# Performance work log

Measured on AMD Instinct MI355X. Metric: run time of the kernel, lower is better.

The kernel has to match this reference:

```python
import jax, jax.numpy as jnp
import numpy as np

B, S, D, H = 2, 2048, 2048, 16
HD = D // H  # head_dim = 128


def setup_inputs() -> dict:
    key = jax.random.key(0)
    k1, k2, k3, k4, k5, k6 = jax.random.split(key, 6)
    scale = 1.0 / np.sqrt(D)
    return {
        "hidden_states": jax.random.normal(k1, (B, S, D), dtype=jnp.float32),
        "attention_mask": jnp.ones((B, S), dtype=jnp.int32),
        "wq": jax.random.normal(k2, (D, D), dtype=jnp.float32) * scale,
        "wk": jax.random.normal(k3, (D, D), dtype=jnp.float32) * scale,
        "wv": jax.random.normal(k4, (D, D), dtype=jnp.float32) * scale,
        "wo": jax.random.normal(k5, (D, D), dtype=jnp.float32) * scale,
        "bo": jax.random.normal(k6, (D,), dtype=jnp.float32) * 0.01,
    }


def reference(hidden_states, attention_mask, wq, wk, wv, wo, bo):
    b, s, d = hidden_states.shape
    # QKV projections (no bias), split heads -> [B, S, H, HD]
    q = (hidden_states @ wq).reshape(b, s, H, HD)
    k = (hidden_states @ wk).reshape(b, s, H, HD)
    v = (hidden_states @ wv).reshape(b, s, H, HD)

    # combined causal + padding mask -> [B, 1, S, S]
    causal = jnp.tril(jnp.ones((s, s), dtype=bool))[None, None]
    pad = (attention_mask > 0)[:, None, None, :]  # [B,1,1,S]
    mask = jnp.logical_and(causal, pad)

    big_neg = jnp.finfo(hidden_states.dtype).min
    bias = jnp.where(mask, 0.0, big_neg).astype(hidden_states.dtype)

    # scaled dot-product attention (flax dot_product_attention scales by 1/sqrt(head_dim))
    scores = jnp.einsum("bqhd,bkhd->bhqk", q, k) / jnp.sqrt(jnp.asarray(HD, hidden_states.dtype))
    probs = jax.nn.softmax(scores + bias, axis=-1)
    ctx = jnp.einsum("bhqk,bkhd->bqhd", probs, v).reshape(b, s, d)

    return ctx @ wo + bo
```

## Files before the change

### kernel.cpp

```cpp
#include <hip/hip_runtime.h>
#include <hip/hip_bf16.h>
#include <stdint.h>

#define Bv 2
#define Sv 2048
#define Dv 2048
#define Hv 16
#define HDv 128
#define Mv (Bv*Sv)

typedef __attribute__((ext_vector_type(8))) short short8;
typedef __attribute__((ext_vector_type(4))) short short4v;
typedef __attribute__((ext_vector_type(4))) float f32x4;

__device__ __forceinline__ unsigned short bf16_rne(float f) {
    union { float f; uint32_t u; } c; c.f = f;
    uint32_t u = c.u;
    u += 0x7fffu + ((u >> 16) & 1u);
    return (unsigned short)(u >> 16);
}

__device__ __forceinline__ uint32_t cvt_pk_bf16(float lo, float hi) {
    uint32_t r;
    asm("v_cvt_pk_bf16_f32 %0, %1, %2" : "=v"(r) : "v"(lo), "v"(hi));
    return r;
}

__device__ __forceinline__ void gload16(const void* g, void* l) {
    __builtin_amdgcn_global_load_lds((const __attribute__((address_space(1))) void*)g,
                                     (__attribute__((address_space(3))) void*)l, 16, 0, 0);
}

__global__ void cvt_x_kernel(const float* __restrict__ x, unsigned short* __restrict__ xb) {
    int i = (blockIdx.x * 256 + threadIdx.x) * 4;
    float4 v = *(const float4*)(x + i);
    short4v o;
    o[0] = (short)bf16_rne(v.x);
    o[1] = (short)bf16_rne(v.y);
    o[2] = (short)bf16_rne(v.z);
    o[3] = (short)bf16_rne(v.w);
    *(short4v*)(xb + i) = o;
}

__global__ void cvt_wt_kernel(const float* __restrict__ w0, const float* __restrict__ w1,
                              const float* __restrict__ w2, const float* __restrict__ w3,
                              unsigned short* __restrict__ wt) {
    __shared__ unsigned short t[64][65];
    int z = blockIdx.z;
    const float* w = (z == 0) ? w0 : (z == 1) ? w1 : (z == 2) ? w2 : w3;
    unsigned short* o = wt + (size_t)z * Dv * Dv;
    int k0 = blockIdx.x * 64, n0 = blockIdx.y * 64;
    for (int i = threadIdx.x; i < 4096; i += 256) {
        int r = i >> 6, c = i & 63;
        t[r][c] = bf16_rne(w[(size_t)(k0 + r) * Dv + n0 + c]);
    }
    __syncthreads();
    for (int i = threadIdx.x; i < 4096; i += 256) {
        int r = i >> 6, c = i & 63;
        o[(size_t)(n0 + r) * Dv + k0 + c] = t[c][r];
    }
}

__global__ void vt_kernel(const unsigned short* __restrict__ V, unsigned short* __restrict__ VT) {
    __shared__ unsigned short t[64 * 64];
    const int tid = threadIdx.x;
    const int b = blockIdx.z;
    const int s0 = blockIdx.x * 64, c0 = blockIdx.y * 64;
    const unsigned short* Vb = V + (size_t)b * Sv * Dv;
    unsigned short* VTb = VT + (size_t)b * Dv * Sv;
    #pragma unroll
    for (int ii = 0; ii < 2; ++ii) {
        int i = tid + ii * 256;
        int r = i >> 3, ch = i & 7;
        short8 v = *(const short8*)&Vb[(size_t)(s0 + r) * Dv + c0 + ch * 8];
        *(short8*)&t[r * 64 + ((ch ^ (r & 7)) << 3)] = v;
    }
    __syncthreads();
    #pragma unroll
    for (int ii = 0; ii < 2; ++ii) {
        int o = tid + ii * 256;
        int orow = o >> 3, och = o & 7;
        short8 v;
        #pragma unroll
        for (int j = 0; j < 8; ++j) {
            int r = och * 8 + j;
            int c = orow;
            v[j] = (short)t[r * 64 + ((((c >> 3) ^ (r & 7)) << 3) | (c & 7))];
        }
        *(short8*)&VTb[(size_t)(c0 + orow) * Sv + s0 + och * 8] = v;
    }
}

template<int FOUT>
__global__ __launch_bounds__(512, 2) void gemm8_kernel(
    const unsigned short* __restrict__ A,
    const unsigned short* __restrict__ WtBase,
    unsigned short* __restrict__ CbBase,
    float* __restrict__ Cf,
    const float* __restrict__ bias,
    int per_xcd_n)
{
    extern __shared__ unsigned short lds[];
    const int tid = threadIdx.x;
    const int wv = tid >> 6, ln = tid & 63;
    const int lr = ln & 15, lg = ln >> 4;
    const int wm = wv >> 2, wn = wv & 3;

    const int bid = blockIdx.x;
    const int xcd = bid & 7, idx = bid >> 3;
    const int n_idx = xcd * per_xcd_n + (idx >> 5);
    const int m_idx = idx & 31;
    const int m0 = m_idx * 128;
    const int n0g = n_idx * 256;
    const int NT = Dv / 64;

    const int srow = ln >> 3;
    const int swz = ((ln & 7) ^ srow) << 3;
    const unsigned short* Ab = A      + (size_t)(m0  + wv * 8 + srow) * Dv + swz;
    const unsigned short* Bb = WtBase + (size_t)(n0g + wv * 8 + srow) * Dv + swz;

    auto STAGE_A = [&](int t, int d) {
        const unsigned short* g = Ab + t * 64;
        #pragma unroll
        for (int j = 0; j < 2; ++j)
            gload16(g + (size_t)(j * 64) * Dv, &lds[d * 24576 + (j * 64 + wv * 8) * 64]);
    };
    auto STAGE_B = [&](int t, int d) {
        const unsigned short* g = Bb + t * 64;
        #pragma unroll
        for (int j = 0; j < 4; ++j)
            gload16(g + (size_t)(j * 64) * Dv, &lds[d * 24576 + 8192 + (j * 64 + wv * 8) * 64]);
    };

    const int aro = (wm * 64 + lr) * 64;
    const int bro = (wn * 64 + lr) * 64;
    const int ach0 = ((lg ^ (lr & 7)) << 3);
    const int ach1 = (((4 + lg) ^ (lr & 7)) << 3);

    f32x4 acc[4][4];
    #pragma unroll
    for (int mi = 0; mi < 4; mi++)
        #pragma unroll
        for (int ni = 0; ni < 4; ni++)
            acc[mi][ni] = (f32x4){0.f, 0.f, 0.f, 0.f};

    STAGE_A(0, 0); STAGE_B(0, 0);
    STAGE_A(1, 1); STAGE_B(1, 1);
    asm volatile("s_waitcnt vmcnt(6)" ::: "memory");
    asm volatile("s_barrier" ::: "memory");

    for (int t = 0; t < NT; ++t) {
        const int d = t % 3, d2 = (t + 2) % 3;
        const unsigned short* la = &lds[d * 24576];
        const unsigned short* lb = &lds[d * 24576 + 8192];

        short8 af[4][2], bf0[2][2];
        #pragma unroll
        for (int mi = 0; mi < 4; mi++) {
            af[mi][0] = *(const short8*)&la[aro + mi * 1024 + ach0];
            af[mi][1] = *(const short8*)&la[aro + mi * 1024 + ach1];
        }
        #pragma unroll
        for (int ni = 0; ni < 2; ni++) {
            bf0[ni][0] = *(const short8*)&lb[bro + ni * 1024 + ach0];
            bf0[ni][1] = *(const short8*)&lb[bro + ni * 1024 + ach1];
        }
        if (t + 2 < NT) STAGE_A(t + 2, d2);
        asm volatile("s_barrier" ::: "memory");
        __builtin_amdgcn_s_setprio(1);
        #pragma unroll
        for (int mi = 0; mi < 4; mi++)
            #pragma unroll
            for (int ni = 0; ni < 2; ni++) {
                acc[mi][ni] = __builtin_amdgcn_mfma_f32_16x16x32_bf16(af[mi][0], bf0[ni][0], acc[mi][ni], 0, 0, 0);
                acc[mi][ni] = __builtin_amdgcn_mfma_f32_16x16x32_bf16(af[mi][1], bf0[ni][1], acc[mi][ni], 0, 0, 0);
            }
        __builtin_amdgcn_s_setprio(0);

        short8 bf1[2][2];
        #pragma unroll
        for (int ni = 0; ni < 2; ni++) {
            bf1[ni][0] = *(const short8*)&lb[bro + (ni + 2) * 1024 + ach0];
            bf1[ni][1] = *(const short8*)&lb[bro + (ni + 2) * 1024 + ach1];
        }
        if (t + 2 < NT) STAGE_B(t + 2, d2);
        asm volatile("s_waitcnt vmcnt(6)" ::: "memory");
        asm volatile("s_barrier" ::: "memory");
        __builtin_amdgcn_s_setprio(1);
        #pragma unroll
        for (int mi = 0; mi < 4; mi++)
            #pragma unroll
            for (int ni = 0; ni < 2; ni++) {
                acc[mi][ni + 2] = __builtin_amdgcn_mfma_f32_16x16x32_bf16(af[mi][0], bf1[ni][0], acc[mi][ni + 2], 0, 0, 0);
                acc[mi][ni + 2] = __builtin_amdgcn_mfma_f32_16x16x32_bf16(af[mi][1], bf1[ni][1], acc[mi][ni + 2], 0, 0, 0);
            }
        __builtin_amdgcn_s_setprio(0);
    }

    if (FOUT) {
        #pragma unroll
        for (int mi = 0; mi < 4; mi++)
            #pragma unroll
            for (int ni = 0; ni < 4; ni++) {
                int row = m0 + wm * 64 + mi * 16 + lg * 4;
                int col = n0g + wn * 64 + ni * 16 + lr;
                float bv = bias[col];
                #pragma unroll
                for (int r = 0; r < 4; r++)
                    Cf[(size_t)(row + r) * Dv + col] = acc[mi][ni][r] + bv;
            }
    } else {
        const int z = n0g >> 11;
        unsigned short* Cz = CbBase + (size_t)z * Mv * Dv;
        const int ncl = (n0g & 2047) + wn * 64;
        #pragma unroll
        for (int mi = 0; mi < 4; mi++)
            #pragma unroll
            for (int ni = 0; ni < 4; ni++) {
                int row = m0 + wm * 64 + mi * 16 + lg * 4;
                int col = ncl + ni * 16 + lr;
                #pragma unroll
                for (int r = 0; r < 4; r++)
                    Cz[(size_t)(row + r) * Dv + col] = bf16_rne(acc[mi][ni][r]);
            }
    }
}

__global__ __launch_bounds__(512) void attn_kernel(
    const unsigned short* __restrict__ Q, const unsigned short* __restrict__ K,
    const unsigned short* __restrict__ VT, const int* __restrict__ pmask,
    unsigned short* __restrict__ CTX)
{
    __shared__ unsigned short lK[2][64 * 128];
    __shared__ unsigned short lVt[2][128 * 64];
    __shared__ int lPmB[2][64];
    __shared__ int lPmOk[2];

    const int tid = threadIdx.x, wv = tid >> 6, ln = tid & 63;
    const int lr = ln & 15, lg = ln >> 4;
    const int L = blockIdx.x;
    const int bh = (L & 7) * 4 + ((L >> 3) & 3);
    const int b = bh >> 4, h = bh & 15;
    const int v = L >> 5;
    const int qidx = (v < 8) ? (15 - v) : (v - 8);
    const int q0 = qidx * 128;
    const int qw0 = q0 + wv * 16;
    const size_t hoff  = (size_t)b * Sv * Dv + (size_t)h * HDv;
    const size_t vtoff = ((size_t)b * Dv + (size_t)h * HDv) * Sv;

    short8 qf[4];
    #pragma unroll
    for (int ds = 0; ds < 4; ds++)
        qf[ds] = *(const short8*)&Q[hoff + (size_t)(qw0 + lr) * Dv + ds * 32 + lg * 8];

    size_t koff[2], voff[2];
    #pragma unroll
    for (int ii = 0; ii < 2; ++ii) {
        int slot = ii * 512 + wv * 64 + ln;
        int krow = slot >> 4, kch = slot & 15;
        koff[ii] = hoff + (size_t)krow * Dv + ((kch ^ (krow & 7)) << 3);
        int vrow = slot >> 3, vch = slot & 7;
        voff[ii] = vtoff + (size_t)vrow * Sv + ((vch ^ (vrow & 7)) << 3);
    }

    auto STAGE = [&](int t, int buf) {
        const size_t kadd = (size_t)(t << 6) * Dv;
        const int vadd = t << 6;
        unsigned short* kb = &lK[buf][0];
        unsigned short* vb = &lVt[buf][0];
        #pragma unroll
        for (int ii = 0; ii < 2; ++ii) {
            gload16(K + koff[ii] + kadd, kb + (ii * 512 + wv * 64) * 8);
            gload16(VT + voff[ii] + vadd, vb + (ii * 512 + wv * 64) * 8);
        }
        if (wv == 0) {
            int pmv = pmask[b * Sv + (t << 6) + ln];
            lPmB[buf][ln] = pmv;
            unsigned long long bal = __ballot(pmv != 0);
            if (ln == 0) lPmOk[buf] = (bal == ~0ull) ? 1 : 0;
        }
    };

    f32x4 acc[8];
    #pragma unroll
    for (int n = 0; n < 8; n++) acc[n] = (f32x4){0.f, 0.f, 0.f, 0.f};
    float mrow = -3.0e38f, lrow = 0.f;
    const float CS = 0.12751744f;
    const int qg = qw0 + lr;
    const int nt = (q0 >> 6) + 2;
    const int srcA = lr + ((lg & 1) << 5);
    const int srcB = srcA + 16;
    const bool hiSel = (lg >= 2);

    auto TILE = [&](int t, int buf, auto CAUSAL_c) {
        constexpr bool CAUSAL = decltype(CAUSAL_c)::value;
        const int kv0 = t << 6;
        const unsigned short* kb = &lK[buf][0];
        const unsigned short* vb = &lVt[buf][0];

        f32x4 st[4];
        #pragma unroll
        for (int t2 = 0; t2 < 4; ++t2) st[t2] = (f32x4){0.f, 0.f, 0.f, 0.f};
        __builtin_amdgcn_s_setprio(1);
        #pragma unroll
        for (int t2 = 0; t2 < 4; ++t2) {
            const int krow = t2 * 16 + lr;
            #pragma unroll
            for (int ds = 0; ds < 4; ++ds) {
                const int ch = ds * 4 + lg;
                short8 kf = *(const short8*)&kb[krow * 128 + ((ch ^ (krow & 7)) << 3)];
                st[t2] = __builtin_amdgcn_mfma_f32_16x16x32_bf16(kf, qf[ds], st[t2], 0, 0, 0);
            }
        }
        __builtin_amdgcn_s_setprio(0);

        float sv[4][4];
        float rmax;
        if constexpr (CAUSAL) {
            const int* pm = &lPmB[buf][0];
            #pragma unroll
            for (int t2 = 0; t2 < 4; ++t2)
                #pragma unroll
                for (int r = 0; r < 4; ++r) {
                    int kvl = t2 * 16 + lg * 4 + r;
                    bool ok = ((kv0 + kvl) <= qg) && (pm[kvl] != 0);
                    sv[t2][r] = ok ? st[t2][r] * CS : -1.0e30f;
                }
            rmax = sv[0][0];
            #pragma unroll
            for (int t2 = 0; t2 < 4; ++t2)
                #pragma unroll
                for (int r = 0; r < 4; ++r) rmax = fmaxf(rmax, sv[t2][r]);
            rmax = fmaxf(rmax, __shfl_xor(rmax, 16, 64));
            rmax = fmaxf(rmax, __shfl_xor(rmax, 32, 64));
        } else {
            rmax = st[0][0];
            #pragma unroll
            for (int t2 = 0; t2 < 4; ++t2)
                #pragma unroll
                for (int r = 0; r < 4; ++r) rmax = fmaxf(rmax, st[t2][r]);
            rmax = fmaxf(rmax, __shfl_xor(rmax, 16, 64));
            rmax = fmaxf(rmax, __shfl_xor(rmax, 32, 64));
            rmax *= CS;
        }

        if (!__all(rmax - mrow <= 8.0f)) {
            float mn = fmaxf(mrow, rmax);
            float alpha = exp2f(mrow - mn);
            mrow = mn;
            lrow *= alpha;
            #pragma unroll
            for (int n = 0; n < 8; n++)
                #pragma unroll
                for (int r = 0; r < 4; r++) acc[n][r] *= alpha;
        }

        float p[4][4]; float psum = 0.f;
        if constexpr (CAUSAL) {
            #pragma unroll
            for (int t2 = 0; t2 < 4; ++t2)
                #pragma unroll
                for (int r = 0; r < 4; ++r) {
                    float e = exp2f(sv[t2][r] - mrow);
                    p[t2][r] = (sv[t2][r] > -5.0e29f) ? e : 0.f;
                    psum += p[t2][r];
                }
        } else {
            if (lPmOk[buf]) {
                #pragma unroll
                for (int t2 = 0; t2 < 4; ++t2)
                    #pragma unroll
                    for (int r = 0; r < 4; ++r) {
                        p[t2][r] = exp2f(fmaf(st[t2][r], CS, -mrow));
                        psum += p[t2][r];
                    }
            } else {
                const int* pm = &lPmB[buf][0];
                #pragma unroll
                for (int t2 = 0; t2 < 4; ++t2)
                    #pragma unroll
                    for (int r = 0; r < 4; ++r) {
                        int kvl = t2 * 16 + lg * 4 + r;
                        float e = exp2f(fmaf(st[t2][r], CS, -mrow));
                        p[t2][r] = (pm[kvl] != 0) ? e : 0.f;
                        psum += p[t2][r];
                    }
            }
        }
        psum += __shfl_xor(psum, 16, 64);
        psum += __shfl_xor(psum, 32, 64);
        lrow += psum;

        uint32_t pk[4][2];
        #pragma unroll
        for (int t2 = 0; t2 < 4; ++t2)
            #pragma unroll
            for (int pp = 0; pp < 2; ++pp)
                pk[t2][pp] = cvt_pk_bf16(p[t2][2 * pp], p[t2][2 * pp + 1]);

        union U { uint32_t u[4]; short8 s; } pa0, pa1;
        {
            uint32_t l0 = (uint32_t)__shfl((int)pk[0][0], srcA, 64), h0 = (uint32_t)__shfl((int)pk[1][0], srcA, 64);
            uint32_t l1 = (uint32_t)__shfl((int)pk[0][1], srcA, 64), h1 = (uint32_t)__shfl((int)pk[1][1], srcA, 64);
            uint32_t l2 = (uint32_t)__shfl((int)pk[0][0], srcB, 64), h2 = (uint32_t)__shfl((int)pk[1][0], srcB, 64);
            uint32_t l3 = (uint32_t)__shfl((int)pk[0][1], srcB, 64), h3 = (uint32_t)__shfl((int)pk[1][1], srcB, 64);
            pa0.u[0] = hiSel ? h0 : l0; pa0.u[1] = hiSel ? h1 : l1;
            pa0.u[2] = hiSel ? h2 : l2; pa0.u[3] = hiSel ? h3 : l3;
        }
        {
            uint32_t l0 = (uint32_t)__shfl((int)pk[2][0], srcA, 64), h0 = (uint32_t)__shfl((int)pk[3][0], srcA, 64);
            uint32_t l1 = (uint32_t)__shfl((int)pk[2][1], srcA, 64), h1 = (uint32_t)__shfl((int)pk[3][1], srcA, 64);
            uint32_t l2 = (uint32_t)__shfl((int)pk[2][0], srcB, 64), h2 = (uint32_t)__shfl((int)pk[3][0], srcB, 64);
            uint32_t l3 = (uint32_t)__shfl((int)pk[2][1], srcB, 64), h3 = (uint32_t)__shfl((int)pk[3][1], srcB, 64);
            pa1.u[0] = hiSel ? h0 : l0; pa1.u[1] = hiSel ? h1 : l1;
            pa1.u[2] = hiSel ? h2 : l2; pa1.u[3] = hiSel ? h3 : l3;
        }

        __builtin_amdgcn_s_setprio(1);
        #pragma unroll
        for (int n = 0; n < 8; n++) {
            const int vrow = n * 16 + lr;
            short8 a0 = *(const short8*)&vb[vrow * 64 + ((lg ^ (vrow & 7)) << 3)];
            acc[n] = __builtin_amdgcn_mfma_f32_16x16x32_bf16(a0, pa0.s, acc[n], 0, 0, 0);
            short8 a1 = *(const short8*)&vb[vrow * 64 + (((4 + lg) ^ (vrow & 7)) << 3)];
            acc[n] = __builtin_amdgcn_mfma_f32_16x16x32_bf16(a1, pa1.s, acc[n], 0, 0, 0);
        }
        __builtin_amdgcn_s_setprio(0);
    };

    STAGE(0, 0);
    __syncthreads();
    int cur = 0;

    for (int t = 0; t < nt; ++t) {
        if (t + 1 < nt) STAGE(t + 1, cur ^ 1);
        const int kv0 = t << 6;
        if (kv0 <= qw0 + 15) {
            if (kv0 + 63 > qw0) TILE(t, cur, std::integral_constant<bool, true>{});
            else                TILE(t, cur, std::integral_constant<bool, false>{});
        }
        __syncthreads();
        cur ^= 1;
    }

    float inv = 1.0f / lrow;
    #pragma unroll
    for (int n = 0; n < 8; n++) {
        short4v o;
        #pragma unroll
        for (int r = 0; r < 4; r++) o[r] = (short)bf16_rne(acc[n][r] * inv);
        *(short4v*)&CTX[hoff + (size_t)qg * Dv + n * 16 + lg * 4] = o;
    }
}

extern "C" void kernel_launch(void* const* d_in, const int* in_sizes, int n_in,
                              void* d_out, int out_size, void* d_ws, size_t ws_size,
                              hipStream_t stream) {
    const float* hs  = (const float*)d_in[0];
    const int*   am  = (const int*)d_in[1];
    const float* wq  = (const float*)d_in[2];
    const float* wk  = (const float*)d_in[3];
    const float* wv_ = (const float*)d_in[4];
    const float* wo  = (const float*)d_in[5];
    const float* bo  = (const float*)d_in[6];
    float* out = (float*)d_out;

    char* ws = (char*)d_ws;
    unsigned short* Xb  = (unsigned short*)ws;
    unsigned short* Wt  = (unsigned short*)(ws + (size_t)16 * 1024 * 1024);
    unsigned short* QKV = (unsigned short*)(ws + (size_t)48 * 1024 * 1024);
    unsigned short* CTX = (unsigned short*)(ws + (size_t)96 * 1024 * 1024);
    unsigned short* VT  = Xb;

    const int LDSB = 3 * 24576 * 2;
    static bool attrSet = false;
    if (!attrSet) {
        hipFuncSetAttribute((const void*)gemm8_kernel<0>, hipFuncAttributeMaxDynamicSharedMemorySize, LDSB);
        hipFuncSetAttribute((const void*)gemm8_kernel<1>, hipFuncAttributeMaxDynamicSharedMemorySize, LDSB);
        attrSet = true;
    }

    hipLaunchKernelGGL(cvt_x_kernel, dim3(Mv * Dv / 4 / 256), dim3(256), 0, stream, hs, Xb);
    hipLaunchKernelGGL(cvt_wt_kernel, dim3(32, 32, 4), dim3(256), 0, stream, wq, wk, wv_, wo, Wt);
    hipLaunchKernelGGL(gemm8_kernel<0>, dim3(768), dim3(512), LDSB, stream,
                       Xb, Wt, QKV, (float*)nullptr, (const float*)nullptr, 3);
    hipLaunchKernelGGL(vt_kernel, dim3(32, 32, 2), dim3(256), 0, stream,
                       QKV + 2 * (size_t)Mv * Dv, VT);
    hipLaunchKernelGGL(attn_kernel, dim3(512), dim3(512), 0, stream,
                       QKV, QKV + (size_t)Mv * Dv, VT, am, CTX);
    hipLaunchKernelGGL(gemm8_kernel<1>, dim3(256), dim3(512), LDSB, stream,
                       CTX, Wt + 3 * (size_t)Dv * Dv, (unsigned short*)nullptr, out, bo, 1);
}
```

Before: 243.1 us.

## Restructure GEMM to 256x256 tiles with K=32 stages, templated on M-block

Replaces the 128x256 GEMM tile with a templated kernel. The QKV projection now uses 256x256 tiles (384 blocks instead of 768), while the output projection keeps 128x256. Each stage now covers K=32 instead of K=64, with a new LDS layout and 4-chunk swizzle. Larger tiles raise arithmetic intensity and cut how often A and B are reloaded, but they double the accumulators for QKV, which risks register pressure and lower occupancy, and the shorter K stages add more barriers per unit of work.

```diff
diff --git a/kernel.cpp b/kernel.cpp
--- a/kernel.cpp
+++ b/kernel.cpp
@@ -91,16 +91,21 @@
     }
 }
 
-template<int FOUT>
-__global__ __launch_bounds__(512, 2) void gemm8_kernel(
+template<int FOUT, int MB>
+__global__ __launch_bounds__(512, 2) void gemm256_kernel(
     const unsigned short* __restrict__ A,
     const unsigned short* __restrict__ WtBase,
     unsigned short* __restrict__ CbBase,
     float* __restrict__ Cf,
     const float* __restrict__ bias,
-    int per_xcd_n)
+    int n_per_xcd, int m_cnt)
 {
+    constexpr int BM   = MB * 32;
+    constexpr int AISS = BM / 128;
+    constexpr int SLOT = (BM + 256) * 32;
+    constexpr int IPT  = AISS + 2;
     extern __shared__ unsigned short lds[];
+
     const int tid = threadIdx.x;
     const int wv = tid >> 6, ln = tid & 63;
     const int lr = ln & 15, lg = ln >> 4;
@@ -108,120 +113,106 @@
 
     const int bid = blockIdx.x;
     const int xcd = bid & 7, idx = bid >> 3;
-    const int n_idx = xcd * per_xcd_n + (idx >> 5);
-    const int m_idx = idx & 31;
-    const int m0 = m_idx * 128;
-    const int n0g = n_idx * 256;
-    const int NT = Dv / 64;
-
-    const int srow = ln >> 3;
-    const int swz = ((ln & 7) ^ srow) << 3;
-    const unsigned short* Ab = A      + (size_t)(m0  + wv * 8 + srow) * Dv + swz;
-    const unsigned short* Bb = WtBase + (size_t)(n0g + wv * 8 + srow) * Dv + swz;
-
-    auto STAGE_A = [&](int t, int d) {
-        const unsigned short* g = Ab + t * 64;
+    const int n_idx = xcd * n_per_xcd + idx / m_cnt;
+    const int m_idx = idx % m_cnt;
+    const int m0 = m_idx * BM, n0g = n_idx * 256;
+    const int NT = Dv / 32;
+
+    const int srow = tid >> 2;
+    const int swzc = ((tid & 3) ^ (srow & 3)) << 3;
+    const unsigned short* Ab = A      + (size_t)(m0  + srow) * Dv + swzc;
+    const unsigned short* Bb = WtBase + (size_t)(n0g + srow) * Dv + swzc;
+
+    auto STAGE_A = [&](int t, int s) {
+        #pragma unroll
+        for (int j = 0; j < AISS; ++j)
+            gload16(Ab + (size_t)(j * 128) * Dv + t * 32, &lds[s * SLOT + (j * 512 + wv * 64) * 8]);
+    };
+    auto STAGE_B = [&](int t, int s) {
         #pragma unroll
         for (int j = 0; j < 2; ++j)
-            gload16(g + (size_t)(j * 64) * Dv, &lds[d * 24576 + (j * 64 + wv * 8) * 64]);
+            gload16(Bb + (size_t)(j * 128) * Dv + t * 32, &lds[s * SLOT + BM * 32 + (j * 512 + wv * 64) * 8]);
     };
-    auto STAGE_B = [&](int t, int d) {
-        const unsigned short* g = Bb + t * 64;
-        #pragma unroll
-        for (int j = 0; j < 4; ++j)
-            gload16(g + (size_t)(j * 64) * Dv, &lds[d * 24576 + 8192 + (j * 64 + wv * 8) * 64]);
-    };
-
-    const int aro = (wm * 64 + lr) * 64;
-    const int bro = (wn * 64 + lr) * 64;
-    const int ach0 = ((lg ^ (lr & 7)) << 3);
-    const int ach1 = (((4 + lg) ^ (lr & 7)) << 3);
-
-    f32x4 acc[4][4];
-    #pragma unroll
-    for (int mi = 0; mi < 4; mi++)
-        #pragma unroll
-        for (int ni = 0; ni < 4; ni++)
-            acc[mi][ni] = (f32x4){0.f, 0.f, 0.f, 0.f};
+
+    const int rch = (lg ^ (lr & 3)) << 3;
+    const int arow0 = wm * (MB * 16) + lr;
+    const int brow0 = wn * 64 + lr;
+
+    f32x4 acc[MB][4];
+    #pragma unroll
+    for (int fm = 0; fm < MB; fm++)
+        #pragma unroll
+        for (int fn = 0; fn < 4; fn++)
+            acc[fm][fn] = (f32x4){0.f, 0.f, 0.f, 0.f};
 
     STAGE_A(0, 0); STAGE_B(0, 0);
     STAGE_A(1, 1); STAGE_B(1, 1);
-    asm volatile("s_waitcnt vmcnt(6)" ::: "memory");
+    asm volatile("s_waitcnt vmcnt(%0)" :: "i"(IPT) : "memory");
     asm volatile("s_barrier" ::: "memory");
 
     for (int t = 0; t < NT; ++t) {
-        const int d = t % 3, d2 = (t + 2) % 3;
-        const unsigned short* la = &lds[d * 24576];
-        const unsigned short* lb = &lds[d * 24576 + 8192];
-
-        short8 af[4][2], bf0[2][2];
-        #pragma unroll
-        for (int mi = 0; mi < 4; mi++) {
-            af[mi][0] = *(const short8*)&la[aro + mi * 1024 + ach0];
-            af[mi][1] = *(const short8*)&la[aro + mi * 1024 + ach1];
-        }
-        #pragma unroll
-        for (int ni = 0; ni < 2; ni++) {
-            bf0[ni][0] = *(const short8*)&lb[bro + ni * 1024 + ach0];
-            bf0[ni][1] = *(const short8*)&lb[bro + ni * 1024 + ach1];
-        }
-        if (t + 2 < NT) STAGE_A(t + 2, d2);
+        const int s = t % 3, s2 = (t + 2) % 3;
+        const unsigned short* la = &lds[s * SLOT];
+        const unsigned short* lb = &lds[s * SLOT + BM * 32];
+
+        short8 a4[4], b4[4];
+        #pragma unroll
+        for (int f = 0; f < 4; ++f) a4[f] = *(const short8*)&la[(arow0 + f * 16) * 32 + rch];
+        #pragma unroll
+        for (int f = 0; f < 4; ++f) b4[f] = *(const short8*)&lb[(brow0 + f * 16) * 32 + rch];
+        if (t + 2 < NT) { STAGE_A(t + 2, s2); if (MB == 4) STAGE_B(t + 2, s2); }
+        if (MB == 4) asm volatile("s_waitcnt vmcnt(%0)" :: "i"(IPT) : "memory");
         asm volatile("s_barrier" ::: "memory");
         __builtin_amdgcn_s_setprio(1);
         #pragma unroll
-        for (int mi = 0; mi < 4; mi++)
-            #pragma unroll
-            for (int ni = 0; ni < 2; ni++) {
-                acc[mi][ni] = __builtin_amdgcn_mfma_f32_16x16x32_bf16(af[mi][0], bf0[ni][0], acc[mi][ni], 0, 0, 0);
-                acc[mi][ni] = __builtin_amdgcn_mfma_f32_16x16x32_bf16(af[mi][1], bf0[ni][1], acc[mi][ni], 0, 0, 0);
-            }
+        for (int fm = 0; fm < 4; ++fm)
+            #pragma unroll
+            for (int fn = 0; fn < 4; ++fn)
+                acc[fm][fn] = __builtin_amdgcn_mfma_f32_16x16x32_bf16(a4[fm], b4[fn], acc[fm][fn], 0, 0, 0);
         __builtin_amdgcn_s_setprio(0);
 
-        short8 bf1[2][2];
-        #pragma unroll
-        for (int ni = 0; ni < 2; ni++) {
-            bf1[ni][0] = *(const short8*)&lb[bro + (ni + 2) * 1024 + ach0];
-            bf1[ni][1] = *(const short8*)&lb[bro + (ni + 2) * 1024 + ach1];
-        }
-        if (t + 2 < NT) STAGE_B(t + 2, d2);
-        asm volatile("s_waitcnt vmcnt(6)" ::: "memory");
-        asm volatile("s_barrier" ::: "memory");
-        __builtin_amdgcn_s_setprio(1);
-        #pragma unroll
-        for (int mi = 0; mi < 4; mi++)
-            #pragma unroll
-            for (int ni = 0; ni < 2; ni++) {
-                acc[mi][ni + 2] = __builtin_amdgcn_mfma_f32_16x16x32_bf16(af[mi][0], bf1[ni][0], acc[mi][ni + 2], 0, 0, 0);
-                acc[mi][ni + 2] = __builtin_amdgcn_mfma_f32_16x16x32_bf16(af[mi][1], bf1[ni][1], acc[mi][ni + 2], 0, 0, 0);
-            }
-        __builtin_amdgcn_s_setprio(0);
+        if (MB == 8) {
+            short8 a8[4];
+            #pragma unroll
+            for (int f = 0; f < 4; ++f) a8[f] = *(const short8*)&la[(arow0 + (4 + f) * 16) * 32 + rch];
+            if (t + 2 < NT) STAGE_B(t + 2, s2);
+            asm volatile("s_waitcnt vmcnt(%0)" :: "i"(IPT) : "memory");
+            asm volatile("s_barrier" ::: "memory");
+            __builtin_amdgcn_s_setprio(1);
+            #pragma unroll
+            for (int fm = 0; fm < 4; ++fm)
+                #pragma unroll
+                for (int fn = 0; fn < 4; ++fn)
+                    acc[4 + fm][fn] = __builtin_amdgcn_mfma_f32_16x16x32_bf16(a8[fm], b4[fn], acc[4 + fm][fn], 0, 0, 0);
+            __builtin_amdgcn_s_setprio(0);
+        }
     }
 
     if (FOUT) {
         #pragma unroll
-        for (int mi = 0; mi < 4; mi++)
-            #pragma unroll
-            for (int ni = 0; ni < 4; ni++) {
-                int row = m0 + wm * 64 + mi * 16 + lg * 4;
-                int col = n0g + wn * 64 + ni * 16 + lr;
+        for (int fm = 0; fm < MB; fm++)
+            #pragma unroll
+            for (int fn = 0; fn < 4; fn++) {
+                int row = m0 + wm * (MB * 16) + fm * 16 + lg * 4;
+                int col = n0g + wn * 64 + fn * 16 + lr;
                 float bv = bias[col];
                 #pragma unroll
                 for (int r = 0; r < 4; r++)
-                    Cf[(size_t)(row + r) * Dv + col] = acc[mi][ni][r] + bv;
+                    Cf[(size_t)(row + r) * Dv + col] = acc[fm][fn][r] + bv;
             }
     } else {
         const int z = n0g >> 11;
         unsigned short* Cz = CbBase + (size_t)z * Mv * Dv;
         const int ncl = (n0g & 2047) + wn * 64;
         #pragma unroll
-        for (int mi = 0; mi < 4; mi++)
-            #pragma unroll
-            for (int ni = 0; ni < 4; ni++) {
-                int row = m0 + wm * 64 + mi * 16 + lg * 4;
-                int col = ncl + ni * 16 + lr;
+        for (int fm = 0; fm < MB; fm++)
+            #pragma unroll
+            for (int fn = 0; fn < 4; fn++) {
+                int row = m0 + wm * (MB * 16) + fm * 16 + lg * 4;
+                int col = ncl + fn * 16 + lr;
                 #pragma unroll
                 for (int r = 0; r < 4; r++)
-                    Cz[(size_t)(row + r) * Dv + col] = bf16_rne(acc[mi][ni][r]);
+                    Cz[(size_t)(row + r) * Dv + col] = bf16_rne(acc[fm][fn][r]);
             }
     }
 }
@@ -472,22 +463,23 @@
     unsigned short* CTX = (unsigned short*)(ws + (size_t)96 * 1024 * 1024);
     unsigned short* VT  = Xb;
 
-    const int LDSB = 3 * 24576 * 2;
+    const int LDSB_QKV = 3 * (256 + 256) * 32 * 2;
+    const int LDSB_OUT = 3 * (128 + 256) * 32 * 2;
     static bool attrSet = false;
     if (!attrSet) {
-        hipFuncSetAttribute((const void*)gemm8_kernel<0>, hipFuncAttributeMaxDynamicSharedMemorySize, LDSB);
-        hipFuncSetAttribute((const void*)gemm8_kernel<1>, hipFuncAttributeMaxDynamicSharedMemorySize, LDSB);
+        hipFuncSetAttribute((const void*)gemm256_kernel<0, 8>, hipFuncAttributeMaxDynamicSharedMemorySize, LDSB_QKV);
+        hipFuncSetAttribute((const void*)gemm256_kernel<1, 4>, hipFuncAttributeMaxDynamicSharedMemorySize, LDSB_OUT);
         attrSet = true;
     }
 
     hipLaunchKernelGGL(cvt_x_kernel, dim3(Mv * Dv / 4 / 256), dim3(256), 0, stream, hs, Xb);
     hipLaunchKernelGGL(cvt_wt_kernel, dim3(32, 32, 4), dim3(256), 0, stream, wq, wk, wv_, wo, Wt);
-    hipLaunchKernelGGL(gemm8_kernel<0>, dim3(768), dim3(512), LDSB, stream,
-                       Xb, Wt, QKV, (float*)nullptr, (const float*)nullptr, 3);
+    hipLaunchKernelGGL((gemm256_kernel<0, 8>), dim3(384), dim3(512), LDSB_QKV, stream,
+                       Xb, Wt, QKV, (float*)nullptr, (const float*)nullptr, 3, 16);
     hipLaunchKernelGGL(vt_kernel, dim3(32, 32, 2), dim3(256), 0, stream,
                        QKV + 2 * (size_t)Mv * Dv, VT);
     hipLaunchKernelGGL(attn_kernel, dim3(512), dim3(512), 0, stream,
                        QKV, QKV + (size_t)Mv * Dv, VT, am, CTX);
-    hipLaunchKernelGGL(gemm8_kernel<1>, dim3(256), dim3(512), LDSB, stream,
-                       CTX, Wt + 3 * (size_t)Dv * Dv, (unsigned short*)nullptr, out, bo, 1);
-}
+    hipLaunchKernelGGL((gemm256_kernel<1, 4>), dim3(256), dim3(512), LDSB_OUT, stream,
+                       CTX, Wt + 3 * (size_t)Dv * Dv, (unsigned short*)nullptr, out, bo, 1, 32);
+}
```

New measurement: 262.6 us. 8.0% more time.

## Use 256x256-tile eight-phase pipelined GEMM for QKV projection

Applied to the files above, without the earlier changes.

Replaces the QKV projection GEMM (128x256 tiles, triple-buffered) with a dedicated kernel using 256x256 output tiles, double-buffered LDS split into half-tile loads, and an eight-phase schedule that interleaves LDS reads, global-to-LDS prefetches and MFMA blocks behind barriers. Larger tiles raise arithmetic intensity and halve the block count to 384. This aims to cut global/LDS traffic per FLOP and hide load latency. The trade-offs are 128 accumulator registers per lane, many more barriers, and 128 KB of LDS per block, which limits occupancy. The output GEMM is de-templated, and its LDS attribute is raised to 144 KB although it still uses about the same buffers.

```diff
diff --git a/kernel.cpp b/kernel.cpp
--- a/kernel.cpp
+++ b/kernel.cpp
@@ -30,6 +30,10 @@
     __builtin_amdgcn_global_load_lds((const __attribute__((address_space(1))) void*)g,
                                      (__attribute__((address_space(3))) void*)l, 16, 0, 0);
 }
+
+#define BARRIER() asm volatile("s_barrier" ::: "memory")
+#define LGKM0()   do { asm volatile("s_waitcnt lgkmcnt(0)" ::: "memory"); \
+                       __builtin_amdgcn_sched_barrier(0); } while (0)
 
 __global__ void cvt_x_kernel(const float* __restrict__ x, unsigned short* __restrict__ xb) {
     int i = (blockIdx.x * 256 + threadIdx.x) * 4;
@@ -91,14 +95,10 @@
     }
 }
 
-template<int FOUT>
-__global__ __launch_bounds__(512, 2) void gemm8_kernel(
+__global__ __launch_bounds__(512, 2) void gemm8ph_kernel(
     const unsigned short* __restrict__ A,
     const unsigned short* __restrict__ WtBase,
-    unsigned short* __restrict__ CbBase,
-    float* __restrict__ Cf,
-    const float* __restrict__ bias,
-    int per_xcd_n)
+    unsigned short* __restrict__ CbBase)
 {
     extern __shared__ unsigned short lds[];
     const int tid = threadIdx.x;
@@ -108,8 +108,153 @@
 
     const int bid = blockIdx.x;
     const int xcd = bid & 7, idx = bid >> 3;
-    const int n_idx = xcd * per_xcd_n + (idx >> 5);
-    const int m_idx = idx & 31;
+    const int n_idx = xcd * 3 + idx / 16;
+    const int m_idx = idx % 16;
+    const int m0 = m_idx * 256, n0g = n_idx * 256;
+
+    const int lrow = wv * 8 + (ln >> 3);
+    const int lcol = ((ln & 7) ^ (ln >> 3)) << 3;
+    const unsigned short* Ag = A      + (size_t)(m0  + lrow) * Dv + lcol;
+    const unsigned short* Bg = WtBase + (size_t)(n0g + lrow) * Dv + lcol;
+
+    auto SH = [&](int T, int isB, int h) {
+        const unsigned short* src = (isB ? Bg : Ag) + (size_t)(h * 128) * Dv + T * 64;
+        unsigned short* dst = &lds[(T & 1) * 32768 + isB * 16384 + h * 8192 + wv * 512];
+        gload16(src, dst);
+        gload16(src + (size_t)64 * Dv, dst + 4096);
+    };
+
+    const int axk = lr & 7;
+    auto RDA = [&](int buf, int fm, int ks) {
+        return *(const short8*)&lds[buf * 32768 + (wm * 128 + fm * 16 + lr) * 64 + (((ks * 4 + lg) ^ axk) << 3)];
+    };
+    auto RDB = [&](int buf, int fn, int ks) {
+        return *(const short8*)&lds[buf * 32768 + 16384 + (wn * 64 + fn * 16 + lr) * 64 + (((ks * 4 + lg) ^ axk) << 3)];
+    };
+
+    f32x4 acc[8][4];
+    #pragma unroll
+    for (int fm = 0; fm < 8; fm++)
+        #pragma unroll
+        for (int fn = 0; fn < 4; fn++)
+            acc[fm][fn] = (f32x4){0.f, 0.f, 0.f, 0.f};
+
+    SH(0, 0, 0); SH(0, 0, 1); SH(0, 1, 0); SH(0, 1, 1);
+    SH(1, 1, 0); SH(1, 0, 0);
+    asm volatile("s_waitcnt vmcnt(4)" ::: "memory");
+    BARRIER();
+
+    short8 af[8], b0[4], b1[4];
+    const int NT2 = 16;
+
+    #define MFMA_BLK(FN0, FN1, BARR) do {                                              \
+        __builtin_amdgcn_s_setprio(1);                                                 \
+        _Pragma("unroll")                                                              \
+        for (int fm = 0; fm < 8; fm++) {                                               \
+            acc[fm][FN0] = __builtin_amdgcn_mfma_f32_16x16x32_bf16(af[fm], BARR[FN0], acc[fm][FN0], 0, 0, 0); \
+            acc[fm][FN1] = __builtin_amdgcn_mfma_f32_16x16x32_bf16(af[fm], BARR[FN1], acc[fm][FN1], 0, 0, 0); \
+        }                                                                              \
+        __builtin_amdgcn_s_setprio(0);                                                 \
+    } while (0)
+
+    for (int i = 0; i < NT2; ++i) {
+        const int Tb = 2 * i + 1;
+        const bool more = (i + 1 < NT2);
+
+        #pragma unroll
+        for (int fm = 0; fm < 8; fm++) af[fm] = RDA(0, fm, 0);
+        #pragma unroll
+        for (int fn = 0; fn < 4; fn++) b0[fn] = RDB(0, fn, 0);
+        SH(Tb, 0, 1);
+        BARRIER(); LGKM0();
+        MFMA_BLK(0, 1, b0);
+        BARRIER();
+
+        #pragma unroll
+        for (int fn = 0; fn < 4; fn++) b1[fn] = RDB(0, fn, 1);
+        SH(Tb, 1, 1);
+        BARRIER(); LGKM0();
+        MFMA_BLK(2, 3, b0);
+        BARRIER();
+
+        #pragma unroll
+        for (int fm = 0; fm < 8; fm++) af[fm] = RDA(0, fm, 1);
+        if (more) SH(Tb + 1, 1, 0);
+        BARRIER(); LGKM0();
+        MFMA_BLK(0, 1, b1);
+        BARRIER();
+
+        if (more) SH(Tb + 1, 0, 0);
+        BARRIER(); LGKM0();
+        MFMA_BLK(2, 3, b1);
+        if (more) asm volatile("s_waitcnt vmcnt(4)" ::: "memory");
+        else      asm volatile("s_waitcnt vmcnt(0)" ::: "memory");
+        BARRIER();
+
+        #pragma unroll
+        for (int fm = 0; fm < 8; fm++) af[fm] = RDA(1, fm, 0);
+        #pragma unroll
+        for (int fn = 0; fn < 4; fn++) b0[fn] = RDB(1, fn, 0);
+        if (more) SH(Tb + 1, 0, 1);
+        BARRIER(); LGKM0();
+        MFMA_BLK(0, 1, b0);
+        BARRIER();
+
+        #pragma unroll
+        for (int fn = 0; fn < 4; fn++) b1[fn] = RDB(1, fn, 1);
+        if (more) SH(Tb + 1, 1, 1);
+        BARRIER(); LGKM0();
+        MFMA_BLK(2, 3, b0);
+        BARRIER();
+
+        #pragma unroll
+        for (int fm = 0; fm < 8; fm++) af[fm] = RDA(1, fm, 1);
+        if (more) SH(Tb + 2, 1, 0);
+        BARRIER(); LGKM0();
+        MFMA_BLK(0, 1, b1);
+        BARRIER();
+
+        if (more) SH(Tb + 2, 0, 0);
+        BARRIER(); LGKM0();
+        MFMA_BLK(2, 3, b1);
+        if (more) {
+            asm volatile("s_waitcnt vmcnt(4)" ::: "memory");
+            BARRIER();
+        }
+    }
+    #undef MFMA_BLK
+
+    const int z = n0g >> 11;
+    unsigned short* Cz = CbBase + (size_t)z * Mv * Dv;
+    const int ncl = (n0g & 2047) + wn * 64;
+    #pragma unroll
+    for (int fm = 0; fm < 8; fm++)
+        #pragma unroll
+        for (int fn = 0; fn < 4; fn++) {
+            int row = m0 + wm * 128 + fm * 16 + lg * 4;
+            int col = ncl + fn * 16 + lr;
+            #pragma unroll
+            for (int r = 0; r < 4; r++)
+                Cz[(size_t)(row + r) * Dv + col] = bf16_rne(acc[fm][fn][r]);
+        }
+}
+
+__global__ __launch_bounds__(512, 2) void gemm8_kernel(
+    const unsigned short* __restrict__ A,
+    const unsigned short* __restrict__ WtBase,
+    float* __restrict__ Cf,
+    const float* __restrict__ bias)
+{
+    extern __shared__ unsigned short lds[];
+    const int tid = threadIdx.x;
+    const int wv = tid >> 6, ln = tid & 63;
+    const int lr = ln & 15, lg = ln >> 4;
+    const int wm = wv >> 2, wn = wv & 3;
+
+    const int bid = blockIdx.x;
+    const int xcd = bid & 7, idx = bid >> 3;
+    const int n_idx = xcd;
+    const int m_idx = idx;
     const int m0 = m_idx * 128;
     const int n0g = n_idx * 256;
     const int NT = Dv / 64;
@@ -147,7 +292,7 @@
     STAGE_A(0, 0); STAGE_B(0, 0);
     STAGE_A(1, 1); STAGE_B(1, 1);
     asm volatile("s_waitcnt vmcnt(6)" ::: "memory");
-    asm volatile("s_barrier" ::: "memory");
+    BARRIER();
 
     for (int t = 0; t < NT; ++t) {
         const int d = t % 3, d2 = (t + 2) % 3;
@@ -166,7 +311,7 @@
             bf0[ni][1] = *(const short8*)&lb[bro + ni * 1024 + ach1];
         }
         if (t + 2 < NT) STAGE_A(t + 2, d2);
-        asm volatile("s_barrier" ::: "memory");
+        BARRIER();
         __builtin_amdgcn_s_setprio(1);
         #pragma unroll
         for (int mi = 0; mi < 4; mi++)
@@ -185,7 +330,7 @@
         }
         if (t + 2 < NT) STAGE_B(t + 2, d2);
         asm volatile("s_waitcnt vmcnt(6)" ::: "memory");
-        asm volatile("s_barrier" ::: "memory");
+        BARRIER();
         __builtin_amdgcn_s_setprio(1);
         #pragma unroll
         for (int mi = 0; mi < 4; mi++)
@@ -197,33 +342,17 @@
         __builtin_amdgcn_s_setprio(0);
     }
 
-    if (FOUT) {
-        #pragma unroll
-        for (int mi = 0; mi < 4; mi++)
-            #pragma unroll
-            for (int ni = 0; ni < 4; ni++) {
-                int row = m0 + wm * 64 + mi * 16 + lg * 4;
-                int col = n0g + wn * 64 + ni * 16 + lr;
-                float bv = bias[col];
-                #pragma unroll
-                for (int r = 0; r < 4; r++)
-                    Cf[(size_t)(row + r) * Dv + col] = acc[mi][ni][r] + bv;
-            }
-    } else {
-        const int z = n0g >> 11;
-        unsigned short* Cz = CbBase + (size_t)z * Mv * Dv;
-        const int ncl = (n0g & 2047) + wn * 64;
-        #pragma unroll
-        for (int mi = 0; mi < 4; mi++)
-            #pragma unroll
-            for (int ni = 0; ni < 4; ni++) {
-                int row = m0 + wm * 64 + mi * 16 + lg * 4;
-                int col = ncl + ni * 16 + lr;
-                #pragma unroll
-                for (int r = 0; r < 4; r++)
-                    Cz[(size_t)(row + r) * Dv + col] = bf16_rne(acc[mi][ni][r]);
-            }
-    }
+    #pragma unroll
+    for (int mi = 0; mi < 4; mi++)
+        #pragma unroll
+        for (int ni = 0; ni < 4; ni++) {
+            int row = m0 + wm * 64 + mi * 16 + lg * 4;
+            int col = n0g + wn * 64 + ni * 16 + lr;
+            float bv = bias[col];
+            #pragma unroll
+            for (int r = 0; r < 4; r++)
+                Cf[(size_t)(row + r) * Dv + col] = acc[mi][ni][r] + bv;
+        }
 }
 
 __global__ __launch_bounds__(512) void attn_kernel(
@@ -472,22 +601,22 @@
     unsigned short* CTX = (unsigned short*)(ws + (size_t)96 * 1024 * 1024);
     unsigned short* VT  = Xb;
 
-    const int LDSB = 3 * 24576 * 2;
+    const int LDSB_8PH = 131072;
+    const int LDSB_OUT = 147456;
     static bool attrSet = false;
     if (!attrSet) {
-        hipFuncSetAttribute((const void*)gemm8_kernel<0>, hipFuncAttributeMaxDynamicSharedMemorySize, LDSB);
-        hipFuncSetAttribute((const void*)gemm8_kernel<1>, hipFuncAttributeMaxDynamicSharedMemorySize, LDSB);
+        hipFuncSetAttribute((const void*)gemm8ph_kernel, hipFuncAttributeMaxDynamicSharedMemorySize, LDSB_8PH);
+        hipFuncSetAttribute((const void*)gemm8_kernel, hipFuncAttributeMaxDynamicSharedMemorySize, LDSB_OUT);
         attrSet = true;
     }
 
     hipLaunchKernelGGL(cvt_x_kernel, dim3(Mv * Dv / 4 / 256), dim3(256), 0, stream, hs, Xb);
     hipLaunchKernelGGL(cvt_wt_kernel, dim3(32, 32, 4), dim3(256), 0, stream, wq, wk, wv_, wo, Wt);
-    hipLaunchKernelGGL(gemm8_kernel<0>, dim3(768), dim3(512), LDSB, stream,
-                       Xb, Wt, QKV, (float*)nullptr, (const float*)nullptr, 3);
+    hipLaunchKernelGGL(gemm8ph_kernel, dim3(384), dim3(512), LDSB_8PH, stream, Xb, Wt, QKV);
     hipLaunchKernelGGL(vt_kernel, dim3(32, 32, 2), dim3(256), 0, stream,
                        QKV + 2 * (size_t)Mv * Dv, VT);
     hipLaunchKernelGGL(attn_kernel, dim3(512), dim3(512), 0, stream,
                        QKV, QKV + (size_t)Mv * Dv, VT, am, CTX);
-    hipLaunchKernelGGL(gemm8_kernel<1>, dim3(256), dim3(512), LDSB, stream,
-                       CTX, Wt + 3 * (size_t)Dv * Dv, (unsigned short*)nullptr, out, bo, 1);
-}
+    hipLaunchKernelGGL(gemm8_kernel, dim3(256), dim3(512), LDSB_OUT, stream,
+                       CTX, Wt + 3 * (size_t)Dv * Dv, out, bo);
+}
```

New measurement: 249.9 us. +2.8%, slower.

## Add dedicated 256-thread QKV GEMM kernel with K=32 triple-buffered tiles

Applied to the files above, without the earlier changes.

Replaces the templated QKV projection GEMM with a new 4-wave kernel. It uses 128x256 tiles with a K-step of 32 and a 3-slot LDS ring of 72KB, so more blocks can be resident per CU. Each wave computes 128x64 with 8x4 MFMA fragments, and there is one barrier pair per K-step. The output GEMM is specialized to the fp32+bias path. Risks include higher register pressure from 32 accumulators, more loop iterations and barriers, and narrower per-wave B reuse.

```diff
diff --git a/kernel.cpp b/kernel.cpp
--- a/kernel.cpp
+++ b/kernel.cpp
@@ -30,6 +30,10 @@
     __builtin_amdgcn_global_load_lds((const __attribute__((address_space(1))) void*)g,
                                      (__attribute__((address_space(3))) void*)l, 16, 0, 0);
 }
+
+#define BARRIER() asm volatile("s_barrier" ::: "memory")
+#define LGKM0()   do { asm volatile("s_waitcnt lgkmcnt(0)" ::: "memory"); \
+                       __builtin_amdgcn_sched_barrier(0); } while (0)
 
 __global__ void cvt_x_kernel(const float* __restrict__ x, unsigned short* __restrict__ xb) {
     int i = (blockIdx.x * 256 + threadIdx.x) * 4;
@@ -91,14 +95,109 @@
     }
 }
 
-template<int FOUT>
+__global__ __launch_bounds__(256, 2) void gemmP_kernel(
+    const unsigned short* __restrict__ A,
+    const unsigned short* __restrict__ WtBase,
+    unsigned short* __restrict__ CbBase)
+{
+    extern __shared__ unsigned short lds[];
+    constexpr int SLOT = 12288;
+    constexpr int BOFF = 4096;
+    constexpr int NT = Dv / 32;
+
+    const int tid = threadIdx.x;
+    const int wv = tid >> 6, ln = tid & 63;
+    const int lr = ln & 15, lg = ln >> 4;
+
+    const int bid = blockIdx.x;
+    const int xcd = bid & 7, idx = bid >> 3;
+    const int n_idx = xcd * 3 + idx / 32;
+    const int m_idx = idx % 32;
+    const int m0 = m_idx * 128, n0g = n_idx * 256;
+
+    const int srow = wv * 16 + (ln >> 2);
+    const int scol = (((ln & 3) ^ ((srow >> 2) & 3)) << 3);
+    const unsigned short* Ag = A      + (size_t)(m0  + srow) * Dv + scol;
+    const unsigned short* Bg = WtBase + (size_t)(n0g + srow) * Dv + scol;
+
+    auto SA = [&](int t, int j) {
+        gload16(Ag + (size_t)(j * 64) * Dv + t * 32,
+                &lds[(t % 3) * SLOT + j * 2048 + wv * 512]);
+    };
+    auto SB = [&](int t, int j) {
+        gload16(Bg + (size_t)(j * 64) * Dv + t * 32,
+                &lds[(t % 3) * SLOT + BOFF + j * 2048 + wv * 512]);
+    };
+
+    auto RDA = [&](int d, int fm) {
+        int row = fm * 16 + lr;
+        return *(const short8*)&lds[d * SLOT + row * 32 + ((lg ^ ((row >> 2) & 3)) << 3)];
+    };
+    auto RDB = [&](int d, int fn) {
+        int row = wv * 64 + fn * 16 + lr;
+        return *(const short8*)&lds[d * SLOT + BOFF + row * 32 + ((lg ^ ((row >> 2) & 3)) << 3)];
+    };
+
+    f32x4 acc[8][4];
+    #pragma unroll
+    for (int fm = 0; fm < 8; fm++)
+        #pragma unroll
+        for (int fn = 0; fn < 4; fn++)
+            acc[fm][fn] = (f32x4){0.f, 0.f, 0.f, 0.f};
+
+    SA(0, 0); SA(0, 1); SB(0, 0); SB(0, 1); SB(0, 2); SB(0, 3);
+    SA(1, 0); SA(1, 1); SB(1, 0); SB(1, 1); SB(1, 2); SB(1, 3);
+    asm volatile("s_waitcnt vmcnt(6)" ::: "memory");
+    BARRIER();
+
+    for (int t = 0; t < NT; ++t) {
+        const int d = t % 3;
+
+        short8 af[8], b[4];
+        #pragma unroll
+        for (int fm = 0; fm < 8; fm++) af[fm] = RDA(d, fm);
+        #pragma unroll
+        for (int fn = 0; fn < 4; fn++) b[fn] = RDB(d, fn);
+
+        if (t + 2 < NT) {
+            SA(t + 2, 0); SA(t + 2, 1);
+            SB(t + 2, 0); SB(t + 2, 1); SB(t + 2, 2); SB(t + 2, 3);
+        }
+        BARRIER(); LGKM0();
+
+        __builtin_amdgcn_s_setprio(1);
+        #pragma unroll
+        for (int fm = 0; fm < 8; fm++)
+            #pragma unroll
+            for (int fn = 0; fn < 4; fn++)
+                acc[fm][fn] = __builtin_amdgcn_mfma_f32_16x16x32_bf16(af[fm], b[fn], acc[fm][fn], 0, 0, 0);
+        __builtin_amdgcn_s_setprio(0);
+
+        if (t + 2 < NT) asm volatile("s_waitcnt vmcnt(6)" ::: "memory");
+        else            asm volatile("s_waitcnt vmcnt(0)" ::: "memory");
+        BARRIER();
+    }
+
+    const int z = n0g >> 11;
+    unsigned short* Cz = CbBase + (size_t)z * Mv * Dv;
+    const int ncl = (n0g & 2047) + wv * 64;
+    #pragma unroll
+    for (int fm = 0; fm < 8; fm++)
+        #pragma unroll
+        for (int fn = 0; fn < 4; fn++) {
+            int row = m0 + fm * 16 + lg * 4;
+            int col = ncl + fn * 16 + lr;
+            #pragma unroll
+            for (int r = 0; r < 4; r++)
+                Cz[(size_t)(row + r) * Dv + col] = bf16_rne(acc[fm][fn][r]);
+        }
+}
+
 __global__ __launch_bounds__(512, 2) void gemm8_kernel(
     const unsigned short* __restrict__ A,
     const unsigned short* __restrict__ WtBase,
-    unsigned short* __restrict__ CbBase,
     float* __restrict__ Cf,
-    const float* __restrict__ bias,
-    int per_xcd_n)
+    const float* __restrict__ bias)
 {
     extern __shared__ unsigned short lds[];
     const int tid = threadIdx.x;
@@ -108,8 +207,8 @@
 
     const int bid = blockIdx.x;
     const int xcd = bid & 7, idx = bid >> 3;
-    const int n_idx = xcd * per_xcd_n + (idx >> 5);
-    const int m_idx = idx & 31;
+    const int n_idx = xcd;
+    const int m_idx = idx;
     const int m0 = m_idx * 128;
     const int n0g = n_idx * 256;
     const int NT = Dv / 64;
@@ -147,7 +246,7 @@
     STAGE_A(0, 0); STAGE_B(0, 0);
     STAGE_A(1, 1); STAGE_B(1, 1);
     asm volatile("s_waitcnt vmcnt(6)" ::: "memory");
-    asm volatile("s_barrier" ::: "memory");
+    BARRIER();
 
     for (int t = 0; t < NT; ++t) {
         const int d = t % 3, d2 = (t + 2) % 3;
@@ -166,7 +265,7 @@
             bf0[ni][1] = *(const short8*)&lb[bro + ni * 1024 + ach1];
         }
         if (t + 2 < NT) STAGE_A(t + 2, d2);
-        asm volatile("s_barrier" ::: "memory");
+        BARRIER();
         __builtin_amdgcn_s_setprio(1);
         #pragma unroll
         for (int mi = 0; mi < 4; mi++)
@@ -185,7 +284,7 @@
         }
         if (t + 2 < NT) STAGE_B(t + 2, d2);
         asm volatile("s_waitcnt vmcnt(6)" ::: "memory");
-        asm volatile("s_barrier" ::: "memory");
+        BARRIER();
         __builtin_amdgcn_s_setprio(1);
         #pragma unroll
         for (int mi = 0; mi < 4; mi++)
@@ -197,33 +296,17 @@
         __builtin_amdgcn_s_setprio(0);
     }
 
-    if (FOUT) {
-        #pragma unroll
-        for (int mi = 0; mi < 4; mi++)
-            #pragma unroll
-            for (int ni = 0; ni < 4; ni++) {
-                int row = m0 + wm * 64 + mi * 16 + lg * 4;
-                int col = n0g + wn * 64 + ni * 16 + lr;
-                float bv = bias[col];
-                #pragma unroll
-                for (int r = 0; r < 4; r++)
-                    Cf[(size_t)(row + r) * Dv + col] = acc[mi][ni][r] + bv;
-            }
-    } else {
-        const int z = n0g >> 11;
-        unsigned short* Cz = CbBase + (size_t)z * Mv * Dv;
-        const int ncl = (n0g & 2047) + wn * 64;
-        #pragma unroll
-        for (int mi = 0; mi < 4; mi++)
-            #pragma unroll
-            for (int ni = 0; ni < 4; ni++) {
-                int row = m0 + wm * 64 + mi * 16 + lg * 4;
-                int col = ncl + ni * 16 + lr;
-                #pragma unroll
-                for (int r = 0; r < 4; r++)
-                    Cz[(size_t)(row + r) * Dv + col] = bf16_rne(acc[mi][ni][r]);
-            }
-    }
+    #pragma unroll
+    for (int mi = 0; mi < 4; mi++)
+        #pragma unroll
+        for (int ni = 0; ni < 4; ni++) {
+            int row = m0 + wm * 64 + mi * 16 + lg * 4;
+            int col = n0g + wn * 64 + ni * 16 + lr;
+            float bv = bias[col];
+            #pragma unroll
+            for (int r = 0; r < 4; r++)
+                Cf[(size_t)(row + r) * Dv + col] = acc[mi][ni][r] + bv;
+        }
 }
 
 __global__ __launch_bounds__(512) void attn_kernel(
@@ -472,22 +555,22 @@
     unsigned short* CTX = (unsigned short*)(ws + (size_t)96 * 1024 * 1024);
     unsigned short* VT  = Xb;
 
-    const int LDSB = 3 * 24576 * 2;
+    const int LDSB_P   = 73728;
+    const int LDSB_OUT = 147456;
     static bool attrSet = false;
     if (!attrSet) {
-        hipFuncSetAttribute((const void*)gemm8_kernel<0>, hipFuncAttributeMaxDynamicSharedMemorySize, LDSB);
-        hipFuncSetAttribute((const void*)gemm8_kernel<1>, hipFuncAttributeMaxDynamicSharedMemorySize, LDSB);
+        hipFuncSetAttribute((const void*)gemmP_kernel, hipFuncAttributeMaxDynamicSharedMemorySize, LDSB_P);
+        hipFuncSetAttribute((const void*)gemm8_kernel, hipFuncAttributeMaxDynamicSharedMemorySize, LDSB_OUT);
         attrSet = true;
     }
 
     hipLaunchKernelGGL(cvt_x_kernel, dim3(Mv * Dv / 4 / 256), dim3(256), 0, stream, hs, Xb);
     hipLaunchKernelGGL(cvt_wt_kernel, dim3(32, 32, 4), dim3(256), 0, stream, wq, wk, wv_, wo, Wt);
-    hipLaunchKernelGGL(gemm8_kernel<0>, dim3(768), dim3(512), LDSB, stream,
-                       Xb, Wt, QKV, (float*)nullptr, (const float*)nullptr, 3);
+    hipLaunchKernelGGL(gemmP_kernel, dim3(768), dim3(256), LDSB_P, stream, Xb, Wt, QKV);
     hipLaunchKernelGGL(vt_kernel, dim3(32, 32, 2), dim3(256), 0, stream,
                        QKV + 2 * (size_t)Mv * Dv, VT);
     hipLaunchKernelGGL(attn_kernel, dim3(512), dim3(512), 0, stream,
                        QKV, QKV + (size_t)Mv * Dv, VT, am, CTX);
-    hipLaunchKernelGGL(gemm8_kernel<1>, dim3(256), dim3(512), LDSB, stream,
-                       CTX, Wt + 3 * (size_t)Dv * Dv, (unsigned short*)nullptr, out, bo, 1);
-}
+    hipLaunchKernelGGL(gemm8_kernel, dim3(256), dim3(512), LDSB_OUT, stream,
+                       CTX, Wt + 3 * (size_t)Dv * Dv, out, bo);
+}
```

Result: slower. 252.2 us (+3.8%).
